# Kernel tuning notes

Hardware: AMD Instinct MI355X
Metric: run time of the kernel (lower is better)

## Reference

```python
import jax, jax.numpy as jnp
import numpy as np

D_NUM = 4      # domain_num
N_ES = 2       # n_expert_specific per domain
N_SH = 4       # total shared experts (n_expert_shared_list = [1,1,1,1])
DIN = 512      # input_dims
H = 256        # expert_params dims[-1]
B = 16384      # batch
NEG_INF = -jnp.inf


def setup_inputs() -> dict:
    key = jax.random.key(0)
    ks = jax.random.split(key, 10)
    s = 1.0 / np.sqrt(DIN)
    x_list = jax.random.normal(ks[0], (D_NUM + 1, B, DIN), jnp.float32)
    sim_domain = jax.random.randint(ks[1], (D_NUM, 2), 0, D_NUM, jnp.int32)
    W_spec = jax.random.normal(ks[2], (D_NUM, N_ES, DIN, H), jnp.float32) * s
    b_spec = jax.random.normal(ks[3], (D_NUM, N_ES, H), jnp.float32) * 0.01
    W_sh = jax.random.normal(ks[4], (N_SH, DIN, H), jnp.float32) * s
    b_sh = jax.random.normal(ks[5], (N_SH, H), jnp.float32) * 0.01
    W_gate = jax.random.normal(ks[6], (D_NUM, DIN, N_ES + N_SH), jnp.float32) * s
    b_gate = jax.random.normal(ks[7], (D_NUM, N_ES + N_SH), jnp.float32) * 0.01
    W_gate_sh = jax.random.normal(ks[8], (DIN, D_NUM * N_ES + N_SH), jnp.float32) * s
    b_gate_sh = jax.random.normal(ks[9], (D_NUM * N_ES + N_SH,), jnp.float32) * 0.01
    return {"x_list": x_list, "sim_domain": sim_domain, "W_spec": W_spec,
            "b_spec": b_spec, "W_sh": W_sh, "b_sh": b_sh, "W_gate": W_gate,
            "b_gate": b_gate, "W_gate_sh": W_gate_sh, "b_gate_sh": b_gate_sh}


def reference(x_list, sim_domain, W_spec, b_spec, W_sh, b_sh, W_gate, b_gate, W_gate_sh, b_gate_sh):
    xd = x_list[:D_NUM]          # [D, B, DIN] per-domain inputs
    xs = x_list[-1]              # [B, DIN] shared input
    # expert MLPs (single hidden layer, relu, dropout=0/eval)
    spec = jax.nn.relu(jnp.einsum('nbd,nedh->nbeh', xd, W_spec) + b_spec[:, None])  # [D,B,E,H]
    shared = jax.nn.relu(jnp.einsum('bd,edh->beh', xs, W_sh) + b_sh)                # [B,S,H]
    # specific gates: softmax activation inside MLP
    g = jax.nn.softmax(jnp.einsum('nbd,nde->nbe', xd, W_gate) + b_gate[:, None], axis=-1)  # [D,B,E+S]
    # mask shared experts of non-similar domains (expert_ranges[d] = [N_ES + d])
    mem = (sim_domain[:, :, None] == jnp.arange(D_NUM)[None, None, :]).any(axis=1)  # [D,D]
    mask = jnp.concatenate([jnp.zeros((D_NUM, N_ES), jnp.float32),
                            jnp.where(mem, 0.0, NEG_INF)], axis=1)                  # [D,E+S]
    # torch code re-softmaxes the (already softmaxed) gate after adding -inf mask
    g = jax.nn.softmax(g + mask[:, None, :], axis=-1)
    # weighted combine without materializing broadcasted shared experts
    outs = (jnp.einsum('nbe,nbeh->nbh', g[..., :N_ES], spec)
            + jnp.einsum('nbe,beh->nbh', g[..., N_ES:], shared))                    # [D,B,H]
    # shared gate (cur_level < n_level)
    gs = jax.nn.softmax(xs @ W_gate_sh + b_gate_sh, axis=-1)                         # [B,D*E+S]
    all_spec = spec.transpose(1, 0, 2, 3).reshape(spec.shape[1], D_NUM * N_ES, H)    # [B,D*E,H]
    out_sh = (jnp.einsum('be,beh->bh', gs[:, :D_NUM * N_ES], all_spec)
              + jnp.einsum('be,beh->bh', gs[:, D_NUM * N_ES:], shared))             # [B,H]
    return jnp.concatenate([outs, out_sh[None]], axis=0)                             # [D+1,B,H]
```

## Files before the change

### kernel.cpp

```cpp
#include <hip/hip_runtime.h>
#include <cstdint>
#include <cstddef>

#define D_NUM 4
#define N_ES  2
#define N_SH  4
#define DIN   512
#define HDIM  256
#define BB    16384
#define MHALF 8192
#define NMAT  12
#define NGATE 36

typedef __bf16 bf16x8 __attribute__((ext_vector_type(8)));
typedef float  f32x4  __attribute__((ext_vector_type(4)));

__device__ __forceinline__ unsigned short f2bf(float f) {
    union { float f; unsigned u; } v; v.f = f;
    unsigned u = v.u;
    unsigned r = (u + 0x7FFFu + ((u >> 16) & 1u)) >> 16;
    return (unsigned short)r;
}
__device__ __forceinline__ float bf2f(unsigned short u) {
    union { unsigned u; float f; } v; v.u = ((unsigned)u) << 16; return v.f;
}
__device__ __forceinline__ void async16(void* l, const void* g) {
    __builtin_amdgcn_global_load_lds(
        (const __attribute__((address_space(1))) void*)g,
        (__attribute__((address_space(3))) void*)l,
        16, 0, 0);
}

__global__ __launch_bounds__(256) void k_wconv(
    const float* __restrict__ Wspec,
    const float* __restrict__ Wsh,
    unsigned short* __restrict__ WT)
{
    __shared__ unsigned short t[64][65];
    const int mat = blockIdx.z;
    const int k0  = blockIdx.x * 64;
    const int h0  = blockIdx.y * 64;
    const float* src = (mat < 8) ? (Wspec + (size_t)mat * DIN * HDIM)
                                 : (Wsh   + (size_t)(mat - 8) * DIN * HDIM);
    #pragma unroll
    for (int i = 0; i < 16; ++i) {
        int idx = i * 256 + threadIdx.x;
        int r = idx >> 6, c = idx & 63;
        t[r][c] = f2bf(src[(size_t)(k0 + r) * HDIM + h0 + c]);
    }
    __syncthreads();
    #pragma unroll
    for (int i = 0; i < 16; ++i) {
        int idx = i * 256 + threadIdx.x;
        int r = idx >> 6, c = idx & 63;
        WT[(size_t)mat * HDIM * DIN + (size_t)(h0 + r) * DIN + k0 + c] = t[c][r];
    }
}

__global__ __launch_bounds__(256) void k_gwt(
    const float* __restrict__ Wg,
    const float* __restrict__ Wgs,
    float* __restrict__ WgT,
    float* __restrict__ WgsT)
{
    int i = blockIdx.x * 256 + threadIdx.x;
    if (i < 4 * 6 * 512) {
        int n = i / 3072, rem = i % 3072;
        int e = rem >> 9, k = rem & 511;
        WgT[i] = Wg[((size_t)n * DIN + k) * 6 + e];
    }
    if (i < 12 * 512) {
        int e = i >> 9, k = i & 511;
        WgsT[i] = Wgs[(size_t)k * 12 + e];
    }
}

__global__ __launch_bounds__(256) void k_prep(
    const float* __restrict__ x,
    const int*   __restrict__ simdom,
    const float* __restrict__ WgT,
    const float* __restrict__ bg,
    const float* __restrict__ WgsT,
    const float* __restrict__ bgs,
    unsigned short* __restrict__ xbf,
    float* __restrict__ gates)
{
    __shared__ float lgate[4][40];
    const int wave = threadIdx.x >> 6;
    const int lane = threadIdx.x & 63;
    const int row  = blockIdx.x * 4 + wave;
    const int k0   = lane * 8;

    #pragma unroll
    for (int m = 0; m < 5; ++m) {
        const float* xp = x + ((size_t)m * BB + row) * DIN + k0;
        float4 a = ((const float4*)xp)[0], b = ((const float4*)xp)[1];
        union { unsigned short us[8]; uint4 v; } pk;
        pk.us[0]=f2bf(a.x); pk.us[1]=f2bf(a.y); pk.us[2]=f2bf(a.z); pk.us[3]=f2bf(a.w);
        pk.us[4]=f2bf(b.x); pk.us[5]=f2bf(b.y); pk.us[6]=f2bf(b.z); pk.us[7]=f2bf(b.w);
        *(uint4*)(xbf + ((size_t)m * BB + row) * DIN + k0) = pk.v;

        if (m < 4) {
            float z[6];
            #pragma unroll
            for (int e = 0; e < 6; ++e) {
                const float* wp = WgT + ((size_t)(m * 6 + e)) * DIN + k0;
                float4 wa = ((const float4*)wp)[0], wb = ((const float4*)wp)[1];
                z[e] = a.x*wa.x + a.y*wa.y + a.z*wa.z + a.w*wa.w
                     + b.x*wb.x + b.y*wb.y + b.z*wb.z + b.w*wb.w;
            }
            #pragma unroll
            for (int off = 32; off > 0; off >>= 1)
                #pragma unroll
                for (int e = 0; e < 6; ++e) z[e] += __shfl_xor(z[e], off, 64);
            #pragma unroll
            for (int e = 0; e < 6; ++e) z[e] += bg[m * 6 + e];
            float mx = z[0];
            #pragma unroll
            for (int e = 1; e < 6; ++e) mx = fmaxf(mx, z[e]);
            float sum = 0.f;
            #pragma unroll
            for (int e = 0; e < 6; ++e) { z[e] = __expf(z[e] - mx); sum += z[e]; }
            float inv = 1.f / sum;
            #pragma unroll
            for (int e = 0; e < 6; ++e) z[e] *= inv;
            int s0 = simdom[m * 2], s1 = simdom[m * 2 + 1];
            float z2[6];
            z2[0] = z[0]; z2[1] = z[1];
            #pragma unroll
            for (int j = 0; j < 4; ++j)
                z2[2 + j] = (s0 == j || s1 == j) ? z[2 + j] : 0.f;
            {
                float w[6];
                w[0] = z[0]; w[1] = z[1];
                #pragma unroll
                for (int j = 0; j < 4; ++j)
                    w[2 + j] = (s0 == j || s1 == j) ? z[2 + j] : -1e30f;
                float mx2 = w[0];
                #pragma unroll
                for (int e = 1; e < 6; ++e) mx2 = fmaxf(mx2, w[e]);
                float sm = 0.f;
                #pragma unroll
                for (int e = 0; e < 6; ++e) { w[e] = __expf(w[e] - mx2); sm += w[e]; }
                float iv = 1.f / sm;
                if (lane == 0) {
                    #pragma unroll
                    for (int e = 0; e < 6; ++e) lgate[wave][m * 6 + e] = w[e] * iv;
                }
            }
        } else {
            float z[12];
            #pragma unroll
            for (int e = 0; e < 12; ++e) {
                const float* wp = WgsT + (size_t)e * DIN + k0;
                float4 wa = ((const float4*)wp)[0], wb = ((const float4*)wp)[1];
                z[e] = a.x*wa.x + a.y*wa.y + a.z*wa.z + a.w*wa.w
                     + b.x*wb.x + b.y*wb.y + b.z*wb.z + b.w*wb.w;
            }
            #pragma unroll
            for (int off = 32; off > 0; off >>= 1)
                #pragma unroll
                for (int e = 0; e < 12; ++e) z[e] += __shfl_xor(z[e], off, 64);
            #pragma unroll
            for (int e = 0; e < 12; ++e) z[e] += bgs[e];
            float mx = z[0];
            #pragma unroll
            for (int e = 1; e < 12; ++e) mx = fmaxf(mx, z[e]);
            float sum = 0.f;
            #pragma unroll
            for (int e = 0; e < 12; ++e) { z[e] = __expf(z[e] - mx); sum += z[e]; }
            float inv = 1.f / sum;
            if (lane == 0) {
                #pragma unroll
                for (int e = 0; e < 12; ++e) lgate[wave][24 + e] = z[e] * inv;
            }
        }
    }
    if (lane < NGATE) gates[(size_t)row * NGATE + lane] = lgate[wave][lane];
}

__global__ __launch_bounds__(256) void k_gemm(
    const unsigned short* __restrict__ xbf,
    const unsigned short* __restrict__ WT,
    const float* __restrict__ bspec,
    const float* __restrict__ bsh,
    unsigned short* __restrict__ S,
    int row_base)
{
    __shared__ unsigned short lbuf[16384];

    const int tid  = threadIdx.x;
    const int wave = tid >> 6;
    const int lane = tid & 63;
    const int mat  = blockIdx.y >> 1;
    const int hh0  = (blockIdx.y & 1) * 128;
    const int plane = (mat < 8) ? (mat >> 1) : 4;
    const int lrow0 = blockIdx.x * 128;

    const unsigned short* Abase = xbf + ((size_t)plane * BB + row_base + lrow0) * DIN;
    const unsigned short* Bbase = WT + (size_t)mat * HDIM * DIN + (size_t)hh0 * DIN;

    const unsigned short* gb = (wave < 2) ? Abase : Bbase;
    unsigned goff[8];
    unsigned loff[8];
    {
        int cg = (lane & 7) ^ ((lane >> 3) & 7);
        #pragma unroll
        for (int i = 0; i < 8; ++i) {
            int slot = wave * 8 + i;
            int r = (slot & 15) * 8 + (lane >> 3);
            goff[i] = (unsigned)(r * DIN + cg * 8);
            loff[i] = (unsigned)(slot * 512);
        }
    }

    f32x4 acc[4][4];
    #pragma unroll
    for (int t = 0; t < 4; ++t)
        #pragma unroll
        for (int u = 0; u < 4; ++u)
            acc[t][u] = (f32x4){0.f, 0.f, 0.f, 0.f};

    const int wm = wave >> 1, wn = wave & 1;
    const int arow = lane & 15, quad = lane >> 4;
    int aofs[4], bofs[4];
    #pragma unroll
    for (int t = 0; t < 4; ++t) {
        int r = wm * 64 + t * 16 + arow;
        aofs[t] = r * 64 + (quad ^ (r & 7)) * 8;
    }
    #pragma unroll
    for (int u = 0; u < 4; ++u) {
        int r = wn * 64 + u * 16 + arow;
        bofs[u] = 8192 + r * 64 + (quad ^ (r & 7)) * 8;
    }

    for (int ks = 0; ks < 8; ++ks) {
        __syncthreads();
        #pragma unroll
        for (int i = 0; i < 8; ++i) {
            async16(lbuf + loff[i], gb + goff[i]);
            goff[i] += 64;
        }
        __syncthreads();

        #pragma unroll
        for (int s2 = 0; s2 < 2; ++s2) {
            const int sx = s2 * 32;
            bf16x8 af[4], bv[4];
            #pragma unroll
            for (int t = 0; t < 4; ++t) af[t] = *(const bf16x8*)(lbuf + (aofs[t] ^ sx));
            #pragma unroll
            for (int u = 0; u < 4; ++u) bv[u] = *(const bf16x8*)(lbuf + (bofs[u] ^ sx));
            #pragma unroll
            for (int t = 0; t < 4; ++t)
                #pragma unroll
                for (int u = 0; u < 4; ++u)
                    acc[t][u] = __builtin_amdgcn_mfma_f32_16x16x32_bf16(af[t], bv[u], acc[t][u], 0, 0, 0);
        }
    }

    #pragma unroll
    for (int u = 0; u < 4; ++u) {
        const int h = hh0 + wn * 64 + u * 16 + arow;
        const float bias = (mat < 8) ? bspec[mat * HDIM + h] : bsh[(mat - 8) * HDIM + h];
        #pragma unroll
        for (int t = 0; t < 4; ++t) {
            #pragma unroll
            for (int reg = 0; reg < 4; ++reg) {
                int lr = lrow0 + wm * 64 + t * 16 + quad * 4 + reg;
                float v = fmaxf(acc[t][u][reg] + bias, 0.f);
                S[((size_t)mat * MHALF + lr) * HDIM + h] = f2bf(v);
            }
        }
    }
}

__global__ __launch_bounds__(256) void k_comb(
    const unsigned short* __restrict__ S,
    const float* __restrict__ gates,
    float* __restrict__ out,
    int row_base)
{
    const int h = threadIdx.x;
    const int r0 = blockIdx.x * 4;
    #pragma unroll
    for (int rr = 0; rr < 4; ++rr) {
        const int lr = r0 + rr;
        const int grow = row_base + lr;
        const float* g = gates + (size_t)grow * NGATE;
        float s[NMAT];
        #pragma unroll
        for (int mat = 0; mat < NMAT; ++mat)
            s[mat] = bf2f(S[((size_t)mat * MHALF + lr) * HDIM + h]);
        float o4 = 0.f;
        #pragma unroll
        for (int j = 0; j < 8; ++j) o4 += g[24 + j] * s[j];
        #pragma unroll
        for (int e = 0; e < 4; ++e) o4 += g[32 + e] * s[8 + e];
        #pragma unroll
        for (int n = 0; n < 4; ++n) {
            float on = g[n*6+0]*s[n*2] + g[n*6+1]*s[n*2+1]
                     + g[n*6+2]*s[8] + g[n*6+3]*s[9] + g[n*6+4]*s[10] + g[n*6+5]*s[11];
            out[((size_t)n * BB + grow) * HDIM + h] = on;
        }
        out[((size_t)4 * BB + grow) * HDIM + h] = o4;
    }
}

extern "C" void kernel_launch(void* const* d_in, const int* in_sizes, int n_in,
                              void* d_out, int out_size, void* d_ws, size_t ws_size,
                              hipStream_t stream) {
    const float* x      = (const float*)d_in[0];
    const int*   simdom = (const int*)  d_in[1];
    const float* Wspec  = (const float*)d_in[2];
    const float* bspec  = (const float*)d_in[3];
    const float* Wsh    = (const float*)d_in[4];
    const float* bsh    = (const float*)d_in[5];
    const float* Wg     = (const float*)d_in[6];
    const float* bg     = (const float*)d_in[7];
    const float* Wgs    = (const float*)d_in[8];
    const float* bgs    = (const float*)d_in[9];
    float* out = (float*)d_out;

    uint8_t* ws = (uint8_t*)d_ws;
    unsigned short* xbf  = (unsigned short*)(ws);
    unsigned short* WT   = (unsigned short*)(ws + 83886080ull);
    float*          gts  = (float*)(ws + 87031808ull);
    float*          WgT  = (float*)(ws + 89391104ull);
    float*          WgsT = (float*)(ws + 89440256ull);
    unsigned short* S    = (unsigned short*)(ws + 89464832ull);

    k_wconv<<<dim3(8, 4, 12), 256, 0, stream>>>(Wspec, Wsh, WT);
    k_gwt<<<48, 256, 0, stream>>>(Wg, Wgs, WgT, WgsT);
    k_prep<<<BB / 4, 256, 0, stream>>>(x, simdom, WgT, bg, WgsT, bgs, xbf, gts);
    for (int half = 0; half < 2; ++half) {
        int row_base = half * MHALF;
        k_gemm<<<dim3(MHALF / 128, 24), 256, 0, stream>>>(xbf, WT, bspec, bsh, S, row_base);
        k_comb<<<MHALF / 4, 256, 0, stream>>>(S, gts, out, row_base);
    }
}
```

Before: 454.5 us.

## Restructure gate prep: stage rows in LDS, one thread per row-gate dot product

The prep kernel now handles 8 rows per block. It stages each row's fp32 input in shared memory while writing the bf16 copy, then gives each gate logit to a single thread that runs the full 512-length dot product, instead of doing 64-lane shuffle reductions per row. The softmax and masking run once at the end per row. This removes the many cross-lane shuffles but leaves most threads idle during the dot products and adds barriers and LDS traffic.

```diff
diff --git a/kernel.cpp b/kernel.cpp
--- a/kernel.cpp
+++ b/kernel.cpp
@@ -11,6 +11,7 @@
 #define MHALF 8192
 #define NMAT  12
 #define NGATE 36
+#define PR    8
 
 typedef __bf16 bf16x8 __attribute__((ext_vector_type(8)));
 typedef float  f32x4  __attribute__((ext_vector_type(4)));
@@ -85,36 +86,75 @@
     unsigned short* __restrict__ xbf,
     float* __restrict__ gates)
 {
-    __shared__ float lgate[4][40];
-    const int wave = threadIdx.x >> 6;
-    const int lane = threadIdx.x & 63;
-    const int row  = blockIdx.x * 4 + wave;
-    const int k0   = lane * 8;
+    __shared__ float xs[PR][516];
+    __shared__ float lg[PR][36];
+    __shared__ float gout[PR * 36];
+    const int t  = threadIdx.x;
+    const int r0 = blockIdx.x * PR;
 
     #pragma unroll
     for (int m = 0; m < 5; ++m) {
-        const float* xp = x + ((size_t)m * BB + row) * DIN + k0;
-        float4 a = ((const float4*)xp)[0], b = ((const float4*)xp)[1];
-        union { unsigned short us[8]; uint4 v; } pk;
-        pk.us[0]=f2bf(a.x); pk.us[1]=f2bf(a.y); pk.us[2]=f2bf(a.z); pk.us[3]=f2bf(a.w);
-        pk.us[4]=f2bf(b.x); pk.us[5]=f2bf(b.y); pk.us[6]=f2bf(b.z); pk.us[7]=f2bf(b.w);
-        *(uint4*)(xbf + ((size_t)m * BB + row) * DIN + k0) = pk.v;
-
+        const float* xp = x + ((size_t)m * BB + r0) * DIN;
+        float4 va[2], vb[2];
+        #pragma unroll
+        for (int i = 0; i < 2; ++i) {
+            int e8 = (t + 256 * i) * 8;
+            va[i] = *(const float4*)(xp + e8);
+            vb[i] = *(const float4*)(xp + e8 + 4);
+        }
+        __syncthreads();
+        unsigned short* xbp = xbf + ((size_t)m * BB + r0) * DIN;
+        #pragma unroll
+        for (int i = 0; i < 2; ++i) {
+            int e8 = (t + 256 * i) * 8;
+            union { unsigned short us[8]; uint4 v; } pk;
+            pk.us[0] = f2bf(va[i].x); pk.us[1] = f2bf(va[i].y);
+            pk.us[2] = f2bf(va[i].z); pk.us[3] = f2bf(va[i].w);
+            pk.us[4] = f2bf(vb[i].x); pk.us[5] = f2bf(vb[i].y);
+            pk.us[6] = f2bf(vb[i].z); pk.us[7] = f2bf(vb[i].w);
+            *(uint4*)(xbp + e8) = pk.v;
+            int r = e8 >> 9, c = e8 & 511;
+            *(float4*)(&xs[r][c])     = va[i];
+            *(float4*)(&xs[r][c + 4]) = vb[i];
+        }
+        __syncthreads();
         if (m < 4) {
+            if (t < PR * 6) {
+                int r = t / 6, e = t % 6;
+                const float* wp = WgT + ((size_t)(m * 6 + e)) * DIN;
+                f32x4 acc = {0.f, 0.f, 0.f, 0.f};
+                #pragma unroll 8
+                for (int k = 0; k < 512; k += 4) {
+                    float4 xv = *(const float4*)(&xs[r][k]);
+                    float4 wv = *(const float4*)(wp + k);
+                    acc[0] += xv.x * wv.x; acc[1] += xv.y * wv.y;
+                    acc[2] += xv.z * wv.z; acc[3] += xv.w * wv.w;
+                }
+                lg[r][m * 6 + e] = acc[0] + acc[1] + acc[2] + acc[3];
+            }
+        } else {
+            if (t < PR * 12) {
+                int r = t / 12, e = t % 12;
+                const float* wp = WgsT + (size_t)e * DIN;
+                f32x4 acc = {0.f, 0.f, 0.f, 0.f};
+                #pragma unroll 8
+                for (int k = 0; k < 512; k += 4) {
+                    float4 xv = *(const float4*)(&xs[r][k]);
+                    float4 wv = *(const float4*)(wp + k);
+                    acc[0] += xv.x * wv.x; acc[1] += xv.y * wv.y;
+                    acc[2] += xv.z * wv.z; acc[3] += xv.w * wv.w;
+                }
+                lg[r][24 + e] = acc[0] + acc[1] + acc[2] + acc[3];
+            }
+        }
+    }
+    __syncthreads();
+    if (t < PR) {
+        #pragma unroll
+        for (int n = 0; n < 4; ++n) {
             float z[6];
             #pragma unroll
-            for (int e = 0; e < 6; ++e) {
-                const float* wp = WgT + ((size_t)(m * 6 + e)) * DIN + k0;
-                float4 wa = ((const float4*)wp)[0], wb = ((const float4*)wp)[1];
-                z[e] = a.x*wa.x + a.y*wa.y + a.z*wa.z + a.w*wa.w
-                     + b.x*wb.x + b.y*wb.y + b.z*wb.z + b.w*wb.w;
-            }
-            #pragma unroll
-            for (int off = 32; off > 0; off >>= 1)
-                #pragma unroll
-                for (int e = 0; e < 6; ++e) z[e] += __shfl_xor(z[e], off, 64);
-            #pragma unroll
-            for (int e = 0; e < 6; ++e) z[e] += bg[m * 6 + e];
+            for (int e = 0; e < 6; ++e) z[e] = lg[t][n * 6 + e] + bg[n * 6 + e];
             float mx = z[0];
             #pragma unroll
             for (int e = 1; e < 6; ++e) mx = fmaxf(mx, z[e]);
@@ -124,45 +164,26 @@
             float inv = 1.f / sum;
             #pragma unroll
             for (int e = 0; e < 6; ++e) z[e] *= inv;
-            int s0 = simdom[m * 2], s1 = simdom[m * 2 + 1];
-            float z2[6];
-            z2[0] = z[0]; z2[1] = z[1];
+            int s0 = simdom[n * 2], s1 = simdom[n * 2 + 1];
+            float w[6];
+            w[0] = z[0]; w[1] = z[1];
             #pragma unroll
             for (int j = 0; j < 4; ++j)
-                z2[2 + j] = (s0 == j || s1 == j) ? z[2 + j] : 0.f;
-            {
-                float w[6];
-                w[0] = z[0]; w[1] = z[1];
-                #pragma unroll
-                for (int j = 0; j < 4; ++j)
-                    w[2 + j] = (s0 == j || s1 == j) ? z[2 + j] : -1e30f;
-                float mx2 = w[0];
-                #pragma unroll
-                for (int e = 1; e < 6; ++e) mx2 = fmaxf(mx2, w[e]);
-                float sm = 0.f;
-                #pragma unroll
-                for (int e = 0; e < 6; ++e) { w[e] = __expf(w[e] - mx2); sm += w[e]; }
-                float iv = 1.f / sm;
-                if (lane == 0) {
-                    #pragma unroll
-                    for (int e = 0; e < 6; ++e) lgate[wave][m * 6 + e] = w[e] * iv;
-                }
-            }
-        } else {
+                w[2 + j] = (s0 == j || s1 == j) ? z[2 + j] : -1e30f;
+            float mx2 = w[0];
+            #pragma unroll
+            for (int e = 1; e < 6; ++e) mx2 = fmaxf(mx2, w[e]);
+            float sm = 0.f;
+            #pragma unroll
+            for (int e = 0; e < 6; ++e) { w[e] = __expf(w[e] - mx2); sm += w[e]; }
+            float iv = 1.f / sm;
+            #pragma unroll
+            for (int e = 0; e < 6; ++e) gout[t * 36 + n * 6 + e] = w[e] * iv;
+        }
+        {
             float z[12];
             #pragma unroll
-            for (int e = 0; e < 12; ++e) {
-                const float* wp = WgsT + (size_t)e * DIN + k0;
-                float4 wa = ((const float4*)wp)[0], wb = ((const float4*)wp)[1];
-                z[e] = a.x*wa.x + a.y*wa.y + a.z*wa.z + a.w*wa.w
-                     + b.x*wb.x + b.y*wb.y + b.z*wb.z + b.w*wb.w;
-            }
-            #pragma unroll
-            for (int off = 32; off > 0; off >>= 1)
-                #pragma unroll
-                for (int e = 0; e < 12; ++e) z[e] += __shfl_xor(z[e], off, 64);
-            #pragma unroll
-            for (int e = 0; e < 12; ++e) z[e] += bgs[e];
+            for (int e = 0; e < 12; ++e) z[e] = lg[t][24 + e] + bgs[e];
             float mx = z[0];
             #pragma unroll
             for (int e = 1; e < 12; ++e) mx = fmaxf(mx, z[e]);
@@ -170,13 +191,13 @@
             #pragma unroll
             for (int e = 0; e < 12; ++e) { z[e] = __expf(z[e] - mx); sum += z[e]; }
             float inv = 1.f / sum;
-            if (lane == 0) {
-                #pragma unroll
-                for (int e = 0; e < 12; ++e) lgate[wave][24 + e] = z[e] * inv;
-            }
-        }
-    }
-    if (lane < NGATE) gates[(size_t)row * NGATE + lane] = lgate[wave][lane];
+            #pragma unroll
+            for (int e = 0; e < 12; ++e) gout[t * 36 + 24 + e] = z[e] * inv;
+        }
+    }
+    __syncthreads();
+    for (int j = t; j < PR * 36; j += 256)
+        gates[(size_t)r0 * NGATE + j] = gout[j];
 }
 
 __global__ __launch_bounds__(256) void k_gemm(
@@ -333,7 +354,7 @@
 
     k_wconv<<<dim3(8, 4, 12), 256, 0, stream>>>(Wspec, Wsh, WT);
     k_gwt<<<48, 256, 0, stream>>>(Wg, Wgs, WgT, WgsT);
-    k_prep<<<BB / 4, 256, 0, stream>>>(x, simdom, WgT, bg, WgsT, bgs, xbf, gts);
+    k_prep<<<BB / PR, 256, 0, stream>>>(x, simdom, WgT, bg, WgsT, bgs, xbf, gts);
     for (int half = 0; half < 2; ++half) {
         int row_base = half * MHALF;
         k_gemm<<<dim3(MHALF / 128, 24), 256, 0, stream>>>(xbf, WT, bspec, bsh, S, row_base);
```

Result: slower. 541.4 us (+19.1%).
